# Kernel optimization log

Measured on AMD Instinct MI355X. Metric: run time of the kernel, lower is better.

Reference implementation:

```python
import jax, jax.numpy as jnp
import numpy as np
from jax import lax

TOTAL_LENGTH = 1024
EMBED_DIM = 128
GRAPH_DIM = 50257
N_STEP = 128  # min_len
BATCH = 32


def setup_inputs() -> dict:
    key = jax.random.key(0)
    k1, k2, k3, k4, k5, k6, k7 = jax.random.split(key, 7)
    s_e = 1.0 / np.sqrt(EMBED_DIM)
    return {
        "zi": jax.random.randint(k1, (BATCH,), 0, TOTAL_LENGTH),
        "y": jax.random.randint(k2, (BATCH, N_STEP), 0, GRAPH_DIM),
        "latent": jax.random.normal(k3, (TOTAL_LENGTH, EMBED_DIM), dtype=jnp.float32) * s_e,
        "Wt": jax.random.normal(k4, (EMBED_DIM, EMBED_DIM), dtype=jnp.float32) * s_e,
        "bt": jax.random.normal(k5, (EMBED_DIM,), dtype=jnp.float32) * s_e,
        "Wv": jax.random.normal(k6, (GRAPH_DIM, EMBED_DIM), dtype=jnp.float32) * s_e,
        "bv": jax.random.normal(k7, (GRAPH_DIM,), dtype=jnp.float32) * s_e,
    }


def reference(zi, y, latent, Wt, bt, Wv, bv):
    # z0: [B, E] gathered from latent table
    z0 = latent[zi]

    def step(z, _):
        # emit current z, then update: z <- tanh(z + transition(z))
        z_next = jnp.tanh(z + z @ Wt.T + bt)
        return z_next, z

    _, zs = lax.scan(step, z0, None, length=N_STEP)  # [T, B, E]
    zs = jnp.transpose(zs, (1, 0, 2))                # [B, T, E]
    logits = jnp.einsum("bte,ve->btv", zs, Wv) + bv  # [B, T, V]
    ys = jax.nn.log_softmax(logits, axis=-1)
    yp = jnp.take_along_axis(ys, y[:, :, None], axis=-1)[:, :, 0]  # [B, T]
    return yp
```

## Files before the change

kernel.cpp:

```cpp
#include <hip/hip_runtime.h>
#include <hip/hip_bf16.h>

#define EMBED 128
#define TSTEPS 128
#define NBATCH 32
#define VDIM 50257
#define VPAD 50304
#define MROWS 4096
#define NGROUPS 786
#define GRIDX 128
#define GRIDY 16
#define CONV_N4 ((VDIM * EMBED) / 4)
#define CONV_BLOCKS ((CONV_N4 + 255) / 256)

static constexpr float LOG2E = 1.4426950408889634f;
static constexpr float LN2   = 0.6931471805599453f;

__device__ __forceinline__ float fast_exp2(float x) {
#if __has_builtin(__builtin_amdgcn_exp2f)
    return __builtin_amdgcn_exp2f(x);
#else
    return exp2f(x);
#endif
}
__device__ __forceinline__ float fast_log2(float x) {
#if __has_builtin(__builtin_amdgcn_logf)
    return __builtin_amdgcn_logf(x);
#else
    return log2f(x);
#endif
}
__device__ __forceinline__ unsigned short f2bf_raw(float f) {
    __hip_bfloat16 h = __float2bfloat16(f);
    union { __hip_bfloat16 b; unsigned short u; } cvt;
    cvt.b = h;
    return cvt.u;
}
__device__ __forceinline__ float bf_raw2f(unsigned short u) {
    union { unsigned int u; float f; } cvt;
    cvt.u = ((unsigned int)u) << 16;
    return cvt.f;
}

__global__ __launch_bounds__(256) void setup_kernel(const int* __restrict__ zi,
                                                    const float* __restrict__ latent,
                                                    const float* __restrict__ Wt,
                                                    const float* __restrict__ bt,
                                                    const float* __restrict__ Wv,
                                                    const float* __restrict__ bv,
                                                    unsigned short* __restrict__ zsb,
                                                    unsigned short* __restrict__ Wvb,
                                                    float* __restrict__ ebt,
                                                    float* __restrict__ S) {
    if (blockIdx.x >= NBATCH) {
        const int cb = blockIdx.x - NBATCH;
        if (cb == 0) {
#pragma unroll
            for (int i = 0; i < MROWS / 256; i++)
                S[i * 256 + threadIdx.x] = 0.f;
        }
        if (cb == 1) {
            const int base4 = (VDIM * EMBED) / 4;
            const int npad4 = ((VPAD - VDIM) * EMBED) / 4;
            for (int i = threadIdx.x; i < npad4; i += 256)
                reinterpret_cast<ushort4*>(Wvb)[base4 + i] = make_ushort4(0, 0, 0, 0);
        }
        const int idx = cb * 256 + threadIdx.x;
        if (idx < VPAD)
            ebt[idx] = (idx < VDIM) ? fast_exp2(bv[idx] * LOG2E) : 0.f;
        if (idx < CONV_N4) {
            float4 v = reinterpret_cast<const float4*>(Wv)[idx];
            ushort4 o;
            o.x = f2bf_raw(v.x); o.y = f2bf_raw(v.y);
            o.z = f2bf_raw(v.z); o.w = f2bf_raw(v.w);
            reinterpret_cast<ushort4*>(Wvb)[idx] = o;
        }
        return;
    }

    __shared__ float zbuf[2][EMBED];
    __shared__ unsigned short zstash[TSTEPS * EMBED];
    const int b = blockIdx.x;
    const int e = threadIdx.x >> 1;
    const int h = threadIdx.x & 1;

    float4 wrow[16];
    const float4* wt4 = reinterpret_cast<const float4*>(Wt + e * EMBED + h * 64);
#pragma unroll
    for (int i = 0; i < 16; i++) wrow[i] = wt4[i];
    const float bte = bt[e];

    if (h == 0) zbuf[0][e] = latent[zi[b] * EMBED + e];
    __syncthreads();

    int cur = 0;
    for (int t = 0; t < TSTEPS; t++) {
        const float zc = zbuf[cur][e];
        if (h == 0)
            zstash[t * EMBED + e] = f2bf_raw(zc * LOG2E);

        const float4* z4 = reinterpret_cast<const float4*>(&zbuf[cur][h * 64]);
        float4 acc = {0.f, 0.f, 0.f, 0.f};
#pragma unroll
        for (int i = 0; i < 16; i++) {
            float4 zv = z4[i];
            acc.x += zv.x * wrow[i].x;
            acc.y += zv.y * wrow[i].y;
            acc.z += zv.z * wrow[i].z;
            acc.w += zv.w * wrow[i].w;
        }
        float v = acc.x + acc.y + acc.z + acc.w;
        float p = __shfl_xor(v, 1);
        float sA = h ? p : v;
        float sB = h ? v : p;
        float znew = tanhf(((zc + sA) + sB) + bte);
        if (h == 0) zbuf[cur ^ 1][e] = znew;
        __syncthreads();
        cur ^= 1;
    }

    uint4* dst = reinterpret_cast<uint4*>(zsb + (long)b * TSTEPS * EMBED);
    const uint4* src = reinterpret_cast<const uint4*>(zstash);
    for (int i = threadIdx.x; i < TSTEPS * EMBED / 8; i += 256)
        dst[i] = src[i];
}

typedef __attribute__((ext_vector_type(8))) short bfrag;
typedef __attribute__((ext_vector_type(4))) float f32x4;

__global__ __launch_bounds__(256) void gemm_lse_kernel(const unsigned short* __restrict__ zsb,
                                                       const unsigned short* __restrict__ Wvb,
                                                       const float* __restrict__ ebt,
                                                       float* __restrict__ S) {
    __shared__ short ldsb[2][8192];

    const int lane  = threadIdx.x & 63;
    const int wave  = threadIdx.x >> 6;
    const int col16 = lane & 15;
    const int quad  = lane >> 4;
    const int mbase = blockIdx.y * 256 + wave * 64;

    const int x  = blockIdx.x;
    const int g0 = x * 6 + min(x, 18);
    const int g1 = g0 + 6 + (x < 18 ? 1 : 0);

    bfrag a[4][4];
    const short* zss = reinterpret_cast<const short*>(zsb);
#pragma unroll
    for (int s = 0; s < 4; s++)
#pragma unroll
        for (int c = 0; c < 4; c++) {
            const short* p = zss + (long)(mbase + s * 16 + col16) * EMBED + c * 32 + quad * 8;
            a[s][c] = *reinterpret_cast<const bfrag*>(p);
        }

    float sums[16];
#pragma unroll
    for (int i = 0; i < 16; i++) sums[i] = 0.f;

    const short* wvs = reinterpret_cast<const short*>(Wvb);

    auto stage = [&](int buf, int g) {
#pragma unroll
        for (int j = 0; j < 4; j++) {
            const int r   = (wave * 4 + j) * 4 + quad;
            const int swz = col16 ^ (r & 15);
            const short* gp = wvs + (long)(g * 64 + r) * EMBED + swz * 8;
            __builtin_amdgcn_global_load_lds(
                (const __attribute__((address_space(1))) void*)gp,
                (__attribute__((address_space(3))) void*)&ldsb[buf][(wave * 4 + j) * 512],
                16, 0, 0);
        }
    };

    int cur = 0;
    stage(0, g0);

    const f32x4 dzero = {0.f, 0.f, 0.f, 0.f};

    for (int g = g0; g < g1; g++) {
        __syncthreads();
        if (g + 1 < g1) stage(cur ^ 1, g + 1);

        float ebl[4];
#pragma unroll
        for (int c = 0; c < 4; c++) ebl[c] = ebt[g * 64 + c * 16 + col16];

#pragma unroll
        for (int c = 0; c < 4; c++) {
            bfrag bf[4];
#pragma unroll
            for (int kc = 0; kc < 4; kc++)
                bf[kc] = *reinterpret_cast<const bfrag*>(
                    &ldsb[cur][(c * 16 + col16) * 128 + (((kc * 4 + quad) ^ col16) * 8)]);

            f32x4 d[4];
#pragma unroll
            for (int s = 0; s < 4; s++)
                d[s] = __builtin_amdgcn_mfma_f32_16x16x32_bf16(a[s][0], bf[0], dzero, 0, 0, 0);
#pragma unroll
            for (int kc = 1; kc < 4; kc++)
#pragma unroll
                for (int s = 0; s < 4; s++)
                    d[s] = __builtin_amdgcn_mfma_f32_16x16x32_bf16(a[s][kc], bf[kc], d[s], 0, 0, 0);

#pragma unroll
            for (int s = 0; s < 4; s++)
#pragma unroll
                for (int r = 0; r < 4; r++)
                    sums[s * 4 + r] = fmaf(fast_exp2(d[s][r]), ebl[c], sums[s * 4 + r]);
        }
        cur ^= 1;
    }

#pragma unroll
    for (int s = 0; s < 4; s++) {
#pragma unroll
        for (int r = 0; r < 4; r++) {
            float v = sums[s * 4 + r];
            v += __shfl_xor(v, 1);
            v += __shfl_xor(v, 2);
            v += __shfl_xor(v, 4);
            v += __shfl_xor(v, 8);
            if (col16 == 0)
                atomicAdd(&S[mbase + s * 16 + quad * 4 + r], v);
        }
    }
}

__global__ __launch_bounds__(256) void tail_kernel(const unsigned short* __restrict__ zsb,
                                                   const float* __restrict__ Wv,
                                                   const float* __restrict__ bv,
                                                   const int* __restrict__ y,
                                                   const float* __restrict__ S,
                                                   float* __restrict__ out) {
    const int row  = blockIdx.x * 4 + (threadIdx.x >> 6);
    const int lane = threadIdx.x & 63;
    const int yv = y[row];
    const ushort2* zr = reinterpret_cast<const ushort2*>(zsb + (long)row * EMBED);
    const float2*  wr = reinterpret_cast<const float2*>(Wv + (long)yv * EMBED);
    ushort2 z2 = zr[lane];
    float2  w2 = wr[lane];
    float v = bf_raw2f(z2.x) * w2.x + bf_raw2f(z2.y) * w2.y;
    v += __shfl_xor(v, 32);
    v += __shfl_xor(v, 16);
    v += __shfl_xor(v, 8);
    v += __shfl_xor(v, 4);
    v += __shfl_xor(v, 2);
    v += __shfl_xor(v, 1);
    if (lane == 0)
        out[row] = LN2 * (v - fast_log2(S[row])) + bv[yv];
}

extern "C" void kernel_launch(void* const* d_in, const int* in_sizes, int n_in,
                              void* d_out, int out_size, void* d_ws, size_t ws_size,
                              hipStream_t stream) {
    const int*   zi     = (const int*)d_in[0];
    const int*   y      = (const int*)d_in[1];
    const float* latent = (const float*)d_in[2];
    const float* Wt     = (const float*)d_in[3];
    const float* bt     = (const float*)d_in[4];
    const float* Wv     = (const float*)d_in[5];
    const float* bv     = (const float*)d_in[6];
    float* out = (float*)d_out;

    char* ws = (char*)d_ws;
    unsigned short* zsb = (unsigned short*)ws;
    float*          S   = (float*)(ws + (1u << 20));
    float*          ebt = (float*)(ws + (1u << 20) + (64u << 10));
    unsigned short* wvb = (unsigned short*)(ws + (2u << 20));

    setup_kernel<<<NBATCH + CONV_BLOCKS, 256, 0, stream>>>(zi, latent, Wt, bt, Wv, bv,
                                                           zsb, wvb, ebt, S);

    gemm_lse_kernel<<<dim3(GRIDX, GRIDY), 256, 0, stream>>>(zsb, wvb, ebt, S);

    tail_kernel<<<MROWS / 4, 256, 0, stream>>>(zsb, Wv, bv, y, S, out);
}
```

Before: 228.3 us.

## Give each wave a private triple-buffered Wv chunk pipeline and drop block barriers

```diff
diff --git a/kernel.cpp b/kernel.cpp
--- a/kernel.cpp
+++ b/kernel.cpp
@@ -7,11 +7,11 @@
 #define VDIM 50257
 #define VPAD 50304
 #define MROWS 4096
-#define NGROUPS 786
-#define GRIDX 128
-#define GRIDY 16
+#define NCHK (VPAD / 16)
+#define GX 12
+#define GY 64
 #define CONV_N4 ((VDIM * EMBED) / 4)
-#define CONV_BLOCKS ((CONV_N4 + 255) / 256)
+#define CONV_BLOCKS ((CONV_N4 + 127) / 128)
 
 static constexpr float LOG2E = 1.4426950408889634f;
 static constexpr float LN2   = 0.6931471805599453f;
@@ -42,7 +42,11 @@
     return cvt.f;
 }
 
-__global__ __launch_bounds__(256) void setup_kernel(const int* __restrict__ zi,
+#define WAITCNT_VM10 0xF7A
+#define WAITCNT_VM5  0xF75
+#define WAITCNT_VM0  0xF70
+
+__global__ __launch_bounds__(128) void setup_kernel(const int* __restrict__ zi,
                                                     const float* __restrict__ latent,
                                                     const float* __restrict__ Wt,
                                                     const float* __restrict__ bt,
@@ -56,16 +60,16 @@
         const int cb = blockIdx.x - NBATCH;
         if (cb == 0) {
 #pragma unroll
-            for (int i = 0; i < MROWS / 256; i++)
-                S[i * 256 + threadIdx.x] = 0.f;
+            for (int i = 0; i < MROWS / 128; i++)
+                S[i * 128 + threadIdx.x] = 0.f;
         }
         if (cb == 1) {
             const int base4 = (VDIM * EMBED) / 4;
             const int npad4 = ((VPAD - VDIM) * EMBED) / 4;
-            for (int i = threadIdx.x; i < npad4; i += 256)
+            for (int i = threadIdx.x; i < npad4; i += 128)
                 reinterpret_cast<ushort4*>(Wvb)[base4 + i] = make_ushort4(0, 0, 0, 0);
         }
-        const int idx = cb * 256 + threadIdx.x;
+        const int idx = cb * 128 + threadIdx.x;
         if (idx < VPAD)
             ebt[idx] = (idx < VDIM) ? fast_exp2(bv[idx] * LOG2E) : 0.f;
         if (idx < CONV_N4) {
@@ -81,47 +85,55 @@
     __shared__ float zbuf[2][EMBED];
     __shared__ unsigned short zstash[TSTEPS * EMBED];
     const int b = blockIdx.x;
-    const int e = threadIdx.x >> 1;
-    const int h = threadIdx.x & 1;
-
-    float4 wrow[16];
-    const float4* wt4 = reinterpret_cast<const float4*>(Wt + e * EMBED + h * 64);
-#pragma unroll
-    for (int i = 0; i < 16; i++) wrow[i] = wt4[i];
+    const int e = threadIdx.x;
+
+    float4 wrowA[16], wrowB[16];
+    const float4* wt4 = reinterpret_cast<const float4*>(Wt + e * EMBED);
+#pragma unroll
+    for (int i = 0; i < 16; i++) wrowA[i] = wt4[i];
+#pragma unroll
+    for (int i = 0; i < 16; i++) wrowB[i] = wt4[16 + i];
     const float bte = bt[e];
 
-    if (h == 0) zbuf[0][e] = latent[zi[b] * EMBED + e];
+    zbuf[0][e] = latent[zi[b] * EMBED + e];
     __syncthreads();
 
     int cur = 0;
     for (int t = 0; t < TSTEPS; t++) {
         const float zc = zbuf[cur][e];
-        if (h == 0)
-            zstash[t * EMBED + e] = f2bf_raw(zc * LOG2E);
-
-        const float4* z4 = reinterpret_cast<const float4*>(&zbuf[cur][h * 64]);
-        float4 acc = {0.f, 0.f, 0.f, 0.f};
+        zstash[t * EMBED + e] = f2bf_raw(zc * LOG2E);
+
+        const float4* z4 = reinterpret_cast<const float4*>(&zbuf[cur][0]);
+        float4 accA = {0.f, 0.f, 0.f, 0.f};
 #pragma unroll
         for (int i = 0; i < 16; i++) {
             float4 zv = z4[i];
-            acc.x += zv.x * wrow[i].x;
-            acc.y += zv.y * wrow[i].y;
-            acc.z += zv.z * wrow[i].z;
-            acc.w += zv.w * wrow[i].w;
-        }
-        float v = acc.x + acc.y + acc.z + acc.w;
-        float p = __shfl_xor(v, 1);
-        float sA = h ? p : v;
-        float sB = h ? v : p;
-        float znew = tanhf(((zc + sA) + sB) + bte);
-        if (h == 0) zbuf[cur ^ 1][e] = znew;
+            accA.x += zv.x * wrowA[i].x;
+            accA.y += zv.y * wrowA[i].y;
+            accA.z += zv.z * wrowA[i].z;
+            accA.w += zv.w * wrowA[i].w;
+        }
+        float vA = accA.x + accA.y + accA.z + accA.w;
+        float4 accB = {0.f, 0.f, 0.f, 0.f};
+#pragma unroll
+        for (int i = 0; i < 16; i++) {
+            float4 zv = z4[16 + i];
+            accB.x += zv.x * wrowB[i].x;
+            accB.y += zv.y * wrowB[i].y;
+            accB.z += zv.z * wrowB[i].z;
+            accB.w += zv.w * wrowB[i].w;
+        }
+        float vB = accB.x + accB.y + accB.z + accB.w;
+
+        float znew = tanhf(((zc + vA) + vB) + bte);
+        zbuf[cur ^ 1][e] = znew;
         __syncthreads();
         cur ^= 1;
     }
 
     uint4* dst = reinterpret_cast<uint4*>(zsb + (long)b * TSTEPS * EMBED);
     const uint4* src = reinterpret_cast<const uint4*>(zstash);
-    for (int i = threadIdx.x; i < TSTEPS * EMBED / 8; i += 256)
+    for (int i = threadIdx.x; i < TSTEPS * EMBED / 8; i += 128)
         dst[i] = src[i];
 }
 
@@ -132,17 +144,17 @@
                                                        const unsigned short* __restrict__ Wvb,
                                                        const float* __restrict__ ebt,
                                                        float* __restrict__ S) {
-    __shared__ short ldsb[2][8192];
+    __shared__ short ldsw[4][3][2048];
 
     const int lane  = threadIdx.x & 63;
     const int wave  = threadIdx.x >> 6;
     const int col16 = lane & 15;
     const int quad  = lane >> 4;
-    const int mbase = blockIdx.y * 256 + wave * 64;
-
-    const int x  = blockIdx.x;
-    const int g0 = x * 6 + min(x, 18);
-    const int g1 = g0 + 6 + (x < 18 ? 1 : 0);
+    const int mbase = blockIdx.y * 64;
+
+    const int w    = blockIdx.x * 4 + wave;
+    const int c0   = w * 65 + min(w, 24);
+    const int cnt  = 65 + (w < 24 ? 1 : 0);
 
     bfrag a[4][4];
     const short* zss = reinterpret_cast<const short*>(zsb);
@@ -159,59 +171,66 @@
     for (int i = 0; i < 16; i++) sums[i] = 0.f;
 
     const short* wvs = reinterpret_cast<const short*>(Wvb);
-
-    auto stage = [&](int buf, int g) {
+    short* wbase = &ldsw[wave][0][0];
+
+    auto stage = [&](int buf, int chk) {
+        short* dst = wbase + buf * 2048;
 #pragma unroll
         for (int j = 0; j < 4; j++) {
-            const int r   = (wave * 4 + j) * 4 + quad;
-            const int swz = col16 ^ (r & 15);
-            const short* gp = wvs + (long)(g * 64 + r) * EMBED + swz * 8;
+            const int r   = j * 4 + quad;
+            const int swz = col16 ^ r;
+            const short* gp = wvs + (long)(chk * 16 + r) * EMBED + swz * 8;
             __builtin_amdgcn_global_load_lds(
                 (const __attribute__((address_space(1))) void*)gp,
-                (__attribute__((address_space(3))) void*)&ldsb[buf][(wave * 4 + j) * 512],
+                (__attribute__((address_space(3))) void*)(dst + j * 512),
                 16, 0, 0);
         }
     };
 
-    int cur = 0;
-    stage(0, g0);
-
-    const f32x4 dzero = {0.f, 0.f, 0.f, 0.f};
-
-    for (int g = g0; g < g1; g++) {
-        __syncthreads();
-        if (g + 1 < g1) stage(cur ^ 1, g + 1);
-
-        float ebl[4];
-#pragma unroll
-        for (int c = 0; c < 4; c++) ebl[c] = ebt[g * 64 + c * 16 + col16];
-
-#pragma unroll
-        for (int c = 0; c < 4; c++) {
-            bfrag bf[4];
-#pragma unroll
-            for (int kc = 0; kc < 4; kc++)
-                bf[kc] = *reinterpret_cast<const bfrag*>(
-                    &ldsb[cur][(c * 16 + col16) * 128 + (((kc * 4 + quad) ^ col16) * 8)]);
-
-            f32x4 d[4];
+    auto body = [&](int buf, float eb) {
+        const short* src = wbase + buf * 2048;
+        bfrag bf[4];
+#pragma unroll
+        for (int kc = 0; kc < 4; kc++)
+            bf[kc] = *reinterpret_cast<const bfrag*>(
+                src + col16 * 128 + (((kc * 4 + quad) ^ col16) * 8));
+
+        const f32x4 dzero = {0.f, 0.f, 0.f, 0.f};
+        f32x4 d[4];
+#pragma unroll
+        for (int s = 0; s < 4; s++)
+            d[s] = __builtin_amdgcn_mfma_f32_16x16x32_bf16(a[s][0], bf[0], dzero, 0, 0, 0);
+#pragma unroll
+        for (int kc = 1; kc < 4; kc++)
 #pragma unroll
             for (int s = 0; s < 4; s++)
-                d[s] = __builtin_amdgcn_mfma_f32_16x16x32_bf16(a[s][0], bf[0], dzero, 0, 0, 0);
-#pragma unroll
-            for (int kc = 1; kc < 4; kc++)
-#pragma unroll
-                for (int s = 0; s < 4; s++)
-                    d[s] = __builtin_amdgcn_mfma_f32_16x16x32_bf16(a[s][kc], bf[kc], d[s], 0, 0, 0);
-
-#pragma unroll
-            for (int s = 0; s < 4; s++)
-#pragma unroll
-                for (int r = 0; r < 4; r++)
-                    sums[s * 4 + r] = fmaf(fast_exp2(d[s][r]), ebl[c], sums[s * 4 + r]);
-        }
-        cur ^= 1;
-    }
+                d[s] = __builtin_amdgcn_mfma_f32_16x16x32_bf16(a[s][kc], bf[kc], d[s], 0, 0, 0);
+
+#pragma unroll
+        for (int s = 0; s < 4; s++)
+#pragma unroll
+            for (int r = 0; r < 4; r++)
+                sums[s * 4 + r] = fmaf(fast_exp2(d[s][r]), eb, sums[s * 4 + r]);
+    };
+
+    stage(0, c0);
+    float ebl0 = ebt[c0 * 16 + col16];
+    stage(1, c0 + 1);
+    float ebl1 = ebt[(c0 + 1) * 16 + col16];
+
+    int b0 = 0, b1 = 1, b2 = 2;
+    for (int i = 0; i < cnt - 2; i++) {
+        stage(b2, c0 + i + 2);
+        float ebl2 = ebt[(c0 + i + 2) * 16 + col16];
+        __builtin_amdgcn_s_waitcnt(WAITCNT_VM10);
+        body(b0, ebl0);
+        ebl0 = ebl1; ebl1 = ebl2;
+        int tmp = b0; b0 = b1; b1 = b2; b2 = tmp;
+    }
+    __builtin_amdgcn_s_waitcnt(WAITCNT_VM5);
+    body(b0, ebl0);
+    __builtin_amdgcn_s_waitcnt(WAITCNT_VM0);
+    body(b1, ebl1);
 
 #pragma unroll
     for (int s = 0; s < 4; s++) {
@@ -270,10 +289,10 @@
     float*          ebt = (float*)(ws + (1u << 20) + (64u << 10));
     unsigned short* wvb = (unsigned short*)(ws + (2u << 20));
 
-    setup_kernel<<<NBATCH + CONV_BLOCKS, 256, 0, stream>>>(zi, latent, Wt, bt, Wv, bv,
+    setup_kernel<<<NBATCH + CONV_BLOCKS, 128, 0, stream>>>(zi, latent, Wt, bt, Wv, bv,
                                                            zsb, wvb, ebt, S);
 
-    gemm_lse_kernel<<<dim3(GRIDX, GRIDY), 256, 0, stream>>>(zsb, wvb, ebt, S);
+    gemm_lse_kernel<<<dim3(GX, GY), 256, 0, stream>>>(zsb, wvb, ebt, S);
 
     tail_kernel<<<MROWS / 4, 256, 0, stream>>>(zsb, Wv, bv, y, S, out);
 }
```

New measurement: 232.1 us. No clear change (+1.7%).
